# Optimization experiments

Measured on AMD Instinct MI355X. Metric: run time of the kernel, lower is better.

The kernel has to match this reference:

```python
import jax, jax.numpy as jnp
import numpy as np
from jax import lax

B, T, D, H, L = 32, 2048, 256, 256, 2


def setup_inputs() -> dict:
    key = jax.random.key(0)
    ks = jax.random.split(key, 9)
    # nn.Linear(in=D+H, out=H) per gate per layer; store as (L, D+H, H) so y = comb @ W + b.
    # Layer 0 input dim == D == H, so all layers share the (D+H, H) shape.
    s = 1.0 / np.sqrt(D + H)
    def w(k):
        return jax.random.uniform(k, (L, D + H, H), jnp.float32, -s, s)
    def b(k):
        return jax.random.uniform(k, (L, H), jnp.float32, -s, s)
    kx, kwf, kbf, kwi, kbi, kwc, kbc, kwo, kbo = ks
    return {
        "x": jax.random.normal(kx, (B, T, D), jnp.float32),
        "Wf": w(kwf), "bf": b(kbf),
        "Wi": w(kwi), "bi": b(kbi),
        "Wc": w(kwc), "bc": b(kbc),
        "Wo": w(kwo), "bo": b(kbo),
    }


def reference(x, Wf, bf, Wi, bi, Wc, bc, Wo, bo):
    L_ = Wf.shape[0]
    Bm, Tm, _ = x.shape
    Hm = Wf.shape[2]
    h0 = jnp.zeros((L_, Bm, Hm), x.dtype)
    c0 = jnp.zeros((L_, Bm, Hm), x.dtype)

    def step(carry, x_t):
        h, c = carry
        inp = x_t
        hs, cs = [], []
        for l in range(L_):  # fixed small layer count
            comb = jnp.concatenate([inp, h[l]], axis=1)  # (B, D+H)
            f = jax.nn.sigmoid(comb @ Wf[l] + bf[l])
            i = jax.nn.sigmoid(comb @ Wi[l] + bi[l]) * jnp.tanh(comb @ Wc[l] + bc[l])
            o = jax.nn.sigmoid(comb @ Wo[l] + bo[l])
            c_new = f * c[l] + i
            h_new = o + jnp.tanh(c_new)  # faithful to source: additive, not o*tanh(c)
            hs.append(h_new)
            cs.append(c_new)
            inp = h_new
        h = jnp.stack(hs)
        c = jnp.stack(cs)
        return (h, c), h[-1]

    (hT, cT), outs = lax.scan(step, (h0, c0), jnp.swapaxes(x, 0, 1))  # outs: (T, B, H)
    outputs = outs.reshape(-1, outs.shape[-1])  # torch.cat(dim=0) -> (T*B, H)
    return outputs, hT, cT
```

## Files before the change

kernel.cpp:

```cpp
#include <hip/hip_runtime.h>
#include <hip/hip_bf16.h>

#define Bdim 32
#define Tdim 2048
#define Ddim 256
#define Hdim 256
#define Ldim 2
#define NWAVE 64
#define RING 16
#define BH (Bdim*Hdim)

typedef short bf16x8 __attribute__((ext_vector_type(8)));
typedef float f32x4  __attribute__((ext_vector_type(4)));

#define MFMA16(a,b,c) __builtin_amdgcn_mfma_f32_16x16x32_bf16((a),(b),(c),0,0,0)

__device__ __forceinline__ short bf_bits(float f){
  __hip_bfloat16 h = __float2bfloat16(f);
  return (short)__builtin_bit_cast(unsigned short, h);
}
__device__ __forceinline__ float bf_f32(short s){
  return __builtin_bit_cast(float, ((unsigned)(unsigned short)s) << 16);
}
__device__ __forceinline__ void split_pair(float f, short& hi, short& lo){
  short h = bf_bits(f);
  lo = bf_bits(f - bf_f32(h));
  hi = h;
}
__device__ __forceinline__ float sigmoid_f(float x){ return 1.0f/(1.0f + __expf(-x)); }
__device__ __forceinline__ float tanh_f(float x){ return 1.0f - 2.0f/(__expf(2.0f*x) + 1.0f); }

__device__ __forceinline__ f32x4 cload4(const float* p){
  f32x4 r;
  asm volatile("global_load_dwordx4 %0, %1, off sc0 sc1" : "=v"(r) : "v"(p));
  return r;
}
__device__ __forceinline__ void cstore(float* p, float v){
  __hip_atomic_store(p, v, __ATOMIC_RELAXED, __HIP_MEMORY_SCOPE_SYSTEM);
}

__device__ __forceinline__ void waitBoth(const int* pA, const int* pB, int lane){
  const int* base = (lane & 32) ? pB : pA;
  const bool act  = (base != nullptr);
  const int* q    = act ? base + (lane & 31) : nullptr;
  while (true){
    int v = act ? __hip_atomic_load(q, __ATOMIC_RELAXED, __HIP_MEMORY_SCOPE_SYSTEM) : 1;
    if (__all(v != 0)) break;
    __builtin_amdgcn_s_sleep(1);
  }
  asm volatile("" ::: "memory");
}

__global__ void __launch_bounds__(64, 1)
lstm_persist(const float* __restrict__ x,
             const float* __restrict__ Wf, const float* __restrict__ bf,
             const float* __restrict__ Wi, const float* __restrict__ bi,
             const float* __restrict__ Wc, const float* __restrict__ bc,
             const float* __restrict__ Wo, const float* __restrict__ bo,
             float* __restrict__ out,
             int*   __restrict__ flags,
             const float* __restrict__ zbuf,
             float* __restrict__ ring)
{
  const int lane  = threadIdx.x;
  const int bid   = blockIdx.x;
  const int layer = bid & 1;
  const int wid   = bid >> 1;
  const int wg    = wid >> 1;
  const int mt    = wid & 1;

  const int l15 = lane & 15;
  const int kg  = lane >> 4;
  const bool lowhalf = (l15 < 8);
  const int mycol = wg*8 + (l15 & 7);
  const int row   = mt*16 + l15;

  const float* W0 = lowhalf ? Wf : Wi;
  const float* W1 = lowhalf ? Wc : Wo;
  const size_t wbase = (size_t)layer*(Ddim+Hdim)*Hdim + mycol;

  bf16x8 whi[2][16], wlo[2][16];
  #pragma unroll
  for (int nt=0; nt<2; ++nt){
    const float* Wp = nt ? W1 : W0;
    #pragma unroll
    for (int ks=0; ks<16; ++ks){
      bf16x8 h8, l8;
      #pragma unroll
      for (int j=0;j<8;++j){
        const int k = ks*32 + kg*8 + j;
        short hh, ll;
        split_pair(Wp[wbase + (size_t)k*Hdim], hh, ll);
        h8[j]=hh; l8[j]=ll;
      }
      whi[nt][ks]=h8; wlo[nt][ks]=l8;
    }
  }
  const float bias0 = (lowhalf ? bf : bi)[layer*Hdim + mycol];
  const float bias1 = (lowhalf ? bc : bo)[layer*Hdim + mycol];

  const float* xrow = x + (size_t)row*Tdim*Ddim;
  const size_t rowH = (size_t)row*Hdim;

  int* l0f = flags;
  int* l1f = flags + (size_t)Tdim*NWAVE;
  int* myf = layer ? l1f : l0f;

  float cst[4] = {0.f,0.f,0.f,0.f};
  float hv[4];

  for (int t=0; t<Tdim; ++t){
    const float* pa;
    const float* pb;
    const int* wA; const int* wB;
    if (layer==0){
      pa = xrow + (size_t)t*Ddim;
      pb = t ? (ring + (size_t)((t-1)&(RING-1))*BH + rowH) : (zbuf + rowH);
      wA = t ? (l0f + (size_t)(t-1)*NWAVE + mt*32) : nullptr;
      wB = (t>=RING) ? (l1f + (size_t)(t-RING)*NWAVE + mt*32) : nullptr;
    } else {
      pa = ring + (size_t)(t&(RING-1))*BH + rowH;
      pb = t ? (out + (size_t)(t-1)*BH + rowH) : (zbuf + rowH);
      wA = l0f + (size_t)t*NWAVE + mt*32;
      wB = t ? (l1f + (size_t)(t-1)*NWAVE + mt*32) : nullptr;
    }

    f32x4 va[8], vb[8];
    f32x4 wa[8], wb[8];

    if (layer==0){
      #pragma unroll
      for (int ks=0; ks<8; ++ks){
        const float* p = pa + ks*32 + kg*8;
        va[ks] = *reinterpret_cast<const f32x4*>(p);
        vb[ks] = *reinterpret_cast<const f32x4*>(p+4);
      }
    }

    waitBoth(wA, wB, lane);

    if (layer==1){
      #pragma unroll
      for (int ks=0; ks<8; ++ks){
        const float* p = pa + ks*32 + kg*8;
        va[ks] = cload4(p);
        vb[ks] = cload4(p+4);
      }
    }
    #pragma unroll
    for (int ks=0; ks<8; ++ks){
      const float* p = pb + ks*32 + kg*8;
      wa[ks] = cload4(p);
      wb[ks] = cload4(p+4);
    }
    asm volatile("s_waitcnt vmcnt(0)" ::: "memory");
    __builtin_amdgcn_sched_barrier(0);

    f32x4 acc0 = {bias0,bias0,bias0,bias0};
    f32x4 acc1 = {bias1,bias1,bias1,bias1};

    #pragma unroll
    for (int ks=0; ks<16; ++ks){
      const f32x4 u = (ks<8) ? va[ks] : wa[ks-8];
      const f32x4 v = (ks<8) ? vb[ks] : wb[ks-8];
      bf16x8 ahi, alo;
      #pragma unroll
      for (int j=0;j<4;++j){
        short h,l;
        split_pair(u[j],h,l); ahi[j]=h;   alo[j]=l;
        split_pair(v[j],h,l); ahi[j+4]=h; alo[j+4]=l;
      }
      acc0 = MFMA16(ahi, whi[0][ks], acc0);
      acc0 = MFMA16(alo, whi[0][ks], acc0);
      acc0 = MFMA16(ahi, wlo[0][ks], acc0);
      acc1 = MFMA16(ahi, whi[1][ks], acc1);
      acc1 = MFMA16(alo, whi[1][ks], acc1);
      acc1 = MFMA16(ahi, wlo[1][ks], acc1);
    }

    #pragma unroll
    for (int r=0;r<4;++r){
      const float z0  = acc0[r], z1 = acc1[r];
      const float z0o = __shfl_xor(z0, 8, 64);
      const float z1o = __shfl_xor(z1, 8, 64);
      const float zf = lowhalf ? z0  : z0o;
      const float zi = lowhalf ? z0o : z0;
      const float zc = lowhalf ? z1  : z1o;
      const float zo = lowhalf ? z1o : z1;
      const float fg = sigmoid_f(zf);
      const float ig = sigmoid_f(zi) * tanh_f(zc);
      const float og = sigmoid_f(zo);
      const float cn = fg*cst[r] + ig;
      cst[r] = cn;
      hv[r]  = og + tanh_f(cn);
    }

    float* hdst = layer ? (out + (size_t)t*BH) : (ring + (size_t)(t&(RING-1))*BH);
    if (lowhalf){
      #pragma unroll
      for (int r=0;r<4;++r)
        cstore(&hdst[(size_t)(mt*16 + kg*4 + r)*Hdim + mycol], hv[r]);
      if (t == Tdim-1){
        float* hT = out + (size_t)Tdim*BH + (size_t)layer*BH;
        float* cT = hT + (size_t)Ldim*BH;
        #pragma unroll
        for (int r=0;r<4;++r){
          const size_t b = (size_t)(mt*16 + kg*4 + r);
          hT[b*Hdim + mycol] = hv[r];
          cT[b*Hdim + mycol] = cst[r];
        }
      }
    }

    asm volatile("s_waitcnt vmcnt(0)" ::: "memory");
    if (lane==0)
      __hip_atomic_store(myf + (size_t)t*NWAVE + mt*32 + wg, 1,
                         __ATOMIC_RELAXED, __HIP_MEMORY_SCOPE_SYSTEM);
  }
}

extern "C" void kernel_launch(void* const* d_in, const int* in_sizes, int n_in,
                              void* d_out, int out_size, void* d_ws, size_t ws_size,
                              hipStream_t stream)
{
  (void)in_sizes; (void)n_in; (void)out_size; (void)ws_size;
  const float* x  = (const float*)d_in[0];
  const float* Wf = (const float*)d_in[1];
  const float* bf = (const float*)d_in[2];
  const float* Wi = (const float*)d_in[3];
  const float* bi = (const float*)d_in[4];
  const float* Wc = (const float*)d_in[5];
  const float* bc = (const float*)d_in[6];
  const float* Wo = (const float*)d_in[7];
  const float* bo = (const float*)d_in[8];
  float* out = (float*)d_out;

  int*   flags = (int*)d_ws;
  float* zbuf  = (float*)d_ws + (size_t)2*Tdim*NWAVE;
  float* ring  = zbuf + BH;

  const size_t zero_bytes = (size_t)2*Tdim*NWAVE*sizeof(int) + (size_t)BH*sizeof(float);
  hipMemsetAsync(d_ws, 0, zero_bytes, stream);

  lstm_persist<<<dim3(2*NWAVE), dim3(64), 0, stream>>>(
      x, Wf, bf, Wi, bi, Wc, bc, Wo, bo, out, flags, zbuf, ring);
}
```

Baseline: 11.02 ms.

## Exchange hidden states as pre-split bf16 hi/lo planes instead of fp32

Producers now split each new hidden value into bf16 hi and lo parts and publish them as two separate planes. Layer 0 uses a ring of these slots and layer 1 a new double-buffered ring. Consumers load the planes directly as MFMA operands, which removes the per-step fp32-to-bf16 split on the critical recurrent path and keeps the same byte count per load. Both lane halves now store (hi or lo), and layer 1 also writes fp32 output separately. The x input split uses a cheaper truncation-based split, which changes rounding slightly.

New measurement: 8.980 ms. -18.5%, faster.

```diff
diff --git a/kernel.cpp b/kernel.cpp
--- a/kernel.cpp
+++ b/kernel.cpp
@@ -9,9 +9,11 @@
 #define NWAVE 64
 #define RING 16
 #define BH (Bdim*Hdim)
+#define R0SLOT (2*BH)
 
 typedef short bf16x8 __attribute__((ext_vector_type(8)));
 typedef float f32x4  __attribute__((ext_vector_type(4)));
+typedef int   i32x4  __attribute__((ext_vector_type(4)));
 
 #define MFMA16(a,b,c) __builtin_amdgcn_mfma_f32_16x16x32_bf16((a),(b),(c),0,0,0)
 
@@ -27,16 +29,22 @@
   lo = bf_bits(f - bf_f32(h));
   hi = h;
 }
+__device__ __forceinline__ void tsplit(float f, short& hi, short& lo){
+  unsigned u = __builtin_bit_cast(unsigned, f);
+  hi = (short)(u >> 16);
+  float r = __builtin_bit_cast(float, u & 0xffff0000u);
+  lo = (short)(__builtin_bit_cast(unsigned, f - r) >> 16);
+}
 __device__ __forceinline__ float sigmoid_f(float x){ return 1.0f/(1.0f + __expf(-x)); }
 __device__ __forceinline__ float tanh_f(float x){ return 1.0f - 2.0f/(__expf(2.0f*x) + 1.0f); }
 
-__device__ __forceinline__ f32x4 cload4(const float* p){
-  f32x4 r;
+__device__ __forceinline__ bf16x8 cload8bf(const unsigned short* p){
+  i32x4 r;
   asm volatile("global_load_dwordx4 %0, %1, off sc0 sc1" : "=v"(r) : "v"(p));
-  return r;
-}
-__device__ __forceinline__ void cstore(float* p, float v){
-  __hip_atomic_store(p, v, __ATOMIC_RELAXED, __HIP_MEMORY_SCOPE_SYSTEM);
+  return __builtin_bit_cast(bf16x8, r);
+}
+__device__ __forceinline__ void cstore_bf(unsigned short* p, short v){
+  asm volatile("global_store_short %0, %1, off sc0 sc1" :: "v"(p), "v"((int)v) : "memory");
 }
 
 __device__ __forceinline__ void waitBoth(const int* pA, const int* pB, int lane){
@@ -59,8 +67,9 @@
              const float* __restrict__ Wo, const float* __restrict__ bo,
              float* __restrict__ out,
              int*   __restrict__ flags,
-             const float* __restrict__ zbuf,
-             float* __restrict__ ring)
+             unsigned short* __restrict__ zplane,
+             unsigned short* __restrict__ ring0,
+             unsigned short* __restrict__ ring1)
 {
   const int lane  = threadIdx.x;
   const int bid   = blockIdx.x;
@@ -110,30 +119,39 @@
   float hv[4];
 
   for (int t=0; t<Tdim; ++t){
-    const float* pa;
-    const float* pb;
-    const int* wA; const int* wB;
+    const unsigned short *pah, *pal;
+    const unsigned short *pbh, *pbl;
+    const float* pax = nullptr;
+    const int *wA, *wB;
     if (layer==0){
-      pa = xrow + (size_t)t*Ddim;
-      pb = t ? (ring + (size_t)((t-1)&(RING-1))*BH + rowH) : (zbuf + rowH);
+      pax = xrow + (size_t)t*Ddim;
+      if (t){
+        const unsigned short* s = ring0 + (size_t)((t-1)&(RING-1))*R0SLOT + rowH;
+        pbh = s; pbl = s + BH;
+      } else { pbh = zplane + rowH; pbl = zplane + BH + rowH; }
       wA = t ? (l0f + (size_t)(t-1)*NWAVE + mt*32) : nullptr;
       wB = (t>=RING) ? (l1f + (size_t)(t-RING)*NWAVE + mt*32) : nullptr;
+      pah = pal = nullptr;
     } else {
-      pa = ring + (size_t)(t&(RING-1))*BH + rowH;
-      pb = t ? (out + (size_t)(t-1)*BH + rowH) : (zbuf + rowH);
+      const unsigned short* a = ring0 + (size_t)(t&(RING-1))*R0SLOT + rowH;
+      pah = a; pal = a + BH;
+      if (t){
+        const unsigned short* s = ring1 + (size_t)((t-1)&1)*R0SLOT + rowH;
+        pbh = s; pbl = s + BH;
+      } else { pbh = zplane + rowH; pbl = zplane + BH + rowH; }
       wA = l0f + (size_t)t*NWAVE + mt*32;
       wB = t ? (l1f + (size_t)(t-1)*NWAVE + mt*32) : nullptr;
     }
 
-    f32x4 va[8], vb[8];
-    f32x4 wa[8], wb[8];
+    bf16x8 Ah[8], Al[8], Bh[8], Bl[8];
+    f32x4 xu[8], xv[8];
 
     if (layer==0){
       #pragma unroll
       for (int ks=0; ks<8; ++ks){
-        const float* p = pa + ks*32 + kg*8;
-        va[ks] = *reinterpret_cast<const f32x4*>(p);
-        vb[ks] = *reinterpret_cast<const f32x4*>(p+4);
+        const float* p = pax + ks*32 + kg*8;
+        xu[ks] = *reinterpret_cast<const f32x4*>(p);
+        xv[ks] = *reinterpret_cast<const f32x4*>(p+4);
       }
     }
 
@@ -142,40 +160,45 @@
     if (layer==1){
       #pragma unroll
       for (int ks=0; ks<8; ++ks){
-        const float* p = pa + ks*32 + kg*8;
-        va[ks] = cload4(p);
-        vb[ks] = cload4(p+4);
+        Ah[ks] = cload8bf(pah + ks*32 + kg*8);
+        Al[ks] = cload8bf(pal + ks*32 + kg*8);
       }
     }
     #pragma unroll
     for (int ks=0; ks<8; ++ks){
-      const float* p = pb + ks*32 + kg*8;
-      wa[ks] = cload4(p);
-      wb[ks] = cload4(p+4);
+      Bh[ks] = cload8bf(pbh + ks*32 + kg*8);
+      Bl[ks] = cload8bf(pbl + ks*32 + kg*8);
     }
     asm volatile("s_waitcnt vmcnt(0)" ::: "memory");
     __builtin_amdgcn_sched_barrier(0);
 
+    if (layer==0){
+      #pragma unroll
+      for (int ks=0; ks<8; ++ks){
+        bf16x8 h8, l8;
+        #pragma unroll
+        for (int j=0;j<4;++j){
+          short h,l;
+          tsplit(xu[ks][j],h,l); h8[j]=h;   l8[j]=l;
+          tsplit(xv[ks][j],h,l); h8[j+4]=h; l8[j+4]=l;
+        }
+        Ah[ks]=h8; Al[ks]=l8;
+      }
+    }
+
     f32x4 acc0 = {bias0,bias0,bias0,bias0};
     f32x4 acc1 = {bias1,bias1,bias1,bias1};
 
     #pragma unroll
     for (int ks=0; ks<16; ++ks){
-      const f32x4 u = (ks<8) ? va[ks] : wa[ks-8];
-      const f32x4 v = (ks<8) ? vb[ks] : wb[ks-8];
-      bf16x8 ahi, alo;
-      #pragma unroll
-      for (int j=0;j<4;++j){
-        short h,l;
-        split_pair(u[j],h,l); ahi[j]=h;   alo[j]=l;
-        split_pair(v[j],h,l); ahi[j+4]=h; alo[j+4]=l;
-      }
-      acc0 = MFMA16(ahi, whi[0][ks], acc0);
-      acc0 = MFMA16(alo, whi[0][ks], acc0);
-      acc0 = MFMA16(ahi, wlo[0][ks], acc0);
-      acc1 = MFMA16(ahi, whi[1][ks], acc1);
-      acc1 = MFMA16(alo, whi[1][ks], acc1);
-      acc1 = MFMA16(ahi, wlo[1][ks], acc1);
+      const bf16x8 ah = (ks<8) ? Ah[ks] : Bh[ks-8];
+      const bf16x8 al = (ks<8) ? Al[ks] : Bl[ks-8];
+      acc0 = MFMA16(ah, whi[0][ks], acc0);
+      acc0 = MFMA16(al, whi[0][ks], acc0);
+      acc0 = MFMA16(ah, wlo[0][ks], acc0);
+      acc1 = MFMA16(ah, whi[1][ks], acc1);
+      acc1 = MFMA16(al, whi[1][ks], acc1);
+      acc1 = MFMA16(ah, wlo[1][ks], acc1);
     }
 
     #pragma unroll
@@ -195,12 +218,22 @@
       hv[r]  = og + tanh_f(cn);
     }
 
-    float* hdst = layer ? (out + (size_t)t*BH) : (ring + (size_t)(t&(RING-1))*BH);
-    if (lowhalf){
-      #pragma unroll
-      for (int r=0;r<4;++r)
-        cstore(&hdst[(size_t)(mt*16 + kg*4 + r)*Hdim + mycol], hv[r]);
-      if (t == Tdim-1){
+    {
+      unsigned short* base = layer ? (ring1 + (size_t)(t&1)*R0SLOT)
+                                   : (ring0 + (size_t)(t&(RING-1))*R0SLOT);
+      unsigned short* myplane = lowhalf ? base : base + BH;
+      #pragma unroll
+      for (int r=0;r<4;++r){
+        short h,l; split_pair(hv[r],h,l);
+        const short v = lowhalf ? h : l;
+        cstore_bf(&myplane[(size_t)(mt*16 + kg*4 + r)*Hdim + mycol], v);
+      }
+      if (layer==1 && lowhalf){
+        #pragma unroll
+        for (int r=0;r<4;++r)
+          out[(size_t)t*BH + (size_t)(mt*16 + kg*4 + r)*Hdim + mycol] = hv[r];
+      }
+      if (t == Tdim-1 && lowhalf){
         float* hT = out + (size_t)Tdim*BH + (size_t)layer*BH;
         float* cT = hT + (size_t)Ldim*BH;
         #pragma unroll
@@ -235,13 +268,15 @@
   const float* bo = (const float*)d_in[8];
   float* out = (float*)d_out;
 
-  int*   flags = (int*)d_ws;
-  float* zbuf  = (float*)d_ws + (size_t)2*Tdim*NWAVE;
-  float* ring  = zbuf + BH;
-
-  const size_t zero_bytes = (size_t)2*Tdim*NWAVE*sizeof(int) + (size_t)BH*sizeof(float);
+  int* flags = (int*)d_ws;
+  unsigned short* zplane = (unsigned short*)(flags + (size_t)2*Tdim*NWAVE);
+  unsigned short* ring0  = zplane + (size_t)2*BH;
+  unsigned short* ring1  = ring0 + (size_t)RING*R0SLOT;
+
+  const size_t zero_bytes = (size_t)2*Tdim*NWAVE*sizeof(int)
+                          + (size_t)2*BH*sizeof(unsigned short);
   hipMemsetAsync(d_ws, 0, zero_bytes, stream);
 
   lstm_persist<<<dim3(2*NWAVE), dim3(64), 0, stream>>>(
-      x, Wf, bf, Wi, bi, Wc, bc, Wo, bo, out, flags, zbuf, ring);
-}
+      x, Wf, bf, Wi, bi, Wc, bc, Wo, bo, out, flags, zplane, ring0, ring1);
+}
```
